# Kernel optimization log

Hardware: AMD Instinct MI355X
Metric: run time of the kernel (lower is better)

Reference implementation:

```python
import jax, jax.numpy as jnp
import numpy as np

EPS = 1e-5
D = 32          # token embedding dim
HEADS = 8
DH = D // HEADS  # 4


def _layernorm(x, g, b):
    mu = jnp.mean(x, axis=-1, keepdims=True)
    var = jnp.mean(jnp.square(x - mu), axis=-1, keepdims=True)
    return (x - mu) / jnp.sqrt(var + EPS) * g + b


def _mhsa(x, Wqvk, W0):
    # x: [..., t, 32]; Wqvk: [96, 32]; W0: [32, 32]
    qkv = x @ Wqvk.T                                   # [..., t, 96]
    qkv = qkv.reshape(qkv.shape[:-1] + (DH, 3, HEADS))  # (d k h) layout of original rearrange
    q, k, v = qkv[..., 0, :], qkv[..., 1, :], qkv[..., 2, :]  # [..., t, d, h]
    scores = jnp.einsum('...tdh,...sdh->...hts', q, k) * (DH ** -0.5)
    attn = jax.nn.softmax(scores, axis=-1)
    out = jnp.einsum('...hts,...sdh->...thd', attn, v)  # [..., t, h, d]
    out = out.reshape(out.shape[:-2] + (D,))            # (h d) concat order
    return out @ W0.T


def setup_inputs() -> dict:
    key = jax.random.key(0)
    ks = jax.random.split(key, 8)
    B = 256
    s = D ** -0.5
    return {
        'x':       jax.random.normal(ks[0], (B, 3, 32, 32, 32), dtype=jnp.float32),
        'pos_y':   jax.random.normal(ks[1], (3, 32, 32), dtype=jnp.float32) * s,
        'Wqvk_y':  jax.random.normal(ks[2], (3, 3 * D, D), dtype=jnp.float32) * s,
        'W0_y':    jax.random.normal(ks[3], (3, D, D), dtype=jnp.float32) * s,
        'g_y':     jnp.ones((D,), dtype=jnp.float32),
        'b_y':     jnp.zeros((D,), dtype=jnp.float32),
        'Wqvk_x':  jax.random.normal(ks[4], (3, 3 * D, D), dtype=jnp.float32) * s,
        'W0_x':    jax.random.normal(ks[5], (3, D, D), dtype=jnp.float32) * s,
        'g_x':     jnp.ones((D,), dtype=jnp.float32),
        'b_x':     jnp.zeros((D,), dtype=jnp.float32),
    }


def reference(x, pos_y, Wqvk_y, W0_y, g_y, b_y, Wqvk_x, W0_x, g_x, b_x):
    # x: [b, 3, l, w, h] with l=w=h=32. Dropout layers are in eval mode (identity).
    tst = jnp.transpose(x, (0, 1, 4, 2, 3))               # [b, 3, i(=h), t(=l), d(=w)]
    # AbsPosEmb1D per RGB channel: in_ @ pos^T
    emb = jnp.einsum('bcitd,cjd->bcitj', tst, pos_y)      # [b, 3, 32, 32, 32]
    outs = []
    for c in range(3):  # distinct r/g/b weights
        o = _mhsa(emb[:, c], Wqvk_y[c], W0_y[c])
        outs.append(_layernorm(emb[:, c] + o, g_y, b_y))
    x_tmp = jnp.stack(outs, axis=1)                       # [b, 3, i, t, 32]
    x_tmp = jnp.transpose(x_tmp, (0, 1, 3, 4, 2))         # [b, 3, t, 32, i]
    x1 = jax.nn.sigmoid(x_tmp) * x                        # first gating

    # BUG in original second loop: it reuses the stale `emb_y` from the last
    # iteration of the first loop (channel b, i = width-1) for every (i, j).
    emb_last = emb[:, 2, -1]                              # [b, 32, 32]
    ys = []
    for c in range(3):
        o = _mhsa(emb_last, Wqvk_x[c], W0_x[c])
        ys.append(_layernorm(emb_last + o, g_x, b_x))
    tmp2 = jnp.stack(ys, axis=1)                          # [b, 3, t, 32]
    # y stacked over i (constant across i), then permuted to [b,3,32,i,32]
    y_perm = jnp.transpose(tmp2, (0, 1, 3, 2))[:, :, :, None, :]  # [b,3,32,1,32]
    return jax.nn.sigmoid(y_perm) * x1
```

## Files before the change

kernel.cpp:

```cpp
#include <hip/hip_runtime.h>
#include <hip/hip_bf16.h>


using bf16 = __hip_bfloat16;
typedef float v2f __attribute__((ext_vector_type(2)));

__device__ __forceinline__ v2f pk_fma(v2f acc, v2f a, v2f b) {
  asm("v_pk_fma_f32 %0, %1, %2, %0" : "+v"(acc) : "v"(a), "v"(b));
  return acc;
}

struct __align__(16) SMem {
  float psJ[32][36];
  float wqF[96][34];
  float esw[32][36];
  float xs[32][34];
  float qS[32][34];
  float kT[32][36];
  float vT[32][36];
};

__device__ __forceinline__ void load_tables(
    SMem& sm, int tid, const float* __restrict__ xbc, int i,
    const float* __restrict__ pos, const float* __restrict__ wq,
    const float* __restrict__ g, const float* __restrict__ b)
{
  const int t = tid >> 3, dq = tid & 7;
  float xv0 = xbc[(t * 32 + dq * 4 + 0) * 32 + i];
  float xv1 = xbc[(t * 32 + dq * 4 + 1) * 32 + i];
  float xv2 = xbc[(t * 32 + dq * 4 + 2) * 32 + i];
  float xv3 = xbc[(t * 32 + dq * 4 + 3) * 32 + i];
  *(v2f*)&sm.xs[t][dq * 4]     = v2f{xv0, xv1};
  *(v2f*)&sm.xs[t][dq * 4 + 2] = v2f{xv2, xv3};
  {
    const int e = tid * 4;
    float4 p = *(const float4*)&pos[e];
    *(float4*)&sm.psJ[e >> 5][e & 31] = p;
  }
  {
    float wf[12];
    *(float4*)&wf[0] = *(const float4*)&wq[tid * 12];
    *(float4*)&wf[4] = *(const float4*)&wq[tid * 12 + 4];
    *(float4*)&wf[8] = *(const float4*)&wq[tid * 12 + 8];
#pragma unroll
    for (int k = 0; k < 6; ++k) {
      const int e = tid * 12 + 2 * k;
      *(v2f*)&sm.wqF[e >> 5][e & 31] = v2f{wf[2 * k], wf[2 * k + 1]};
    }
  }
  if (tid < 32) { sm.esw[tid][34] = g[tid]; sm.esw[tid][35] = b[tid]; }
}

__device__ __forceinline__ void mhsa_core(SMem& sm, int tid,
                                          const float* __restrict__ w0g,
                                          float sig_out[4])
{
  const int t = tid >> 3, j4 = tid & 7;
  float eres[4];

  {
    v2f acc[4] = {v2f{0.f,0.f}, v2f{0.f,0.f}, v2f{0.f,0.f}, v2f{0.f,0.f}};
#pragma unroll
    for (int d4 = 0; d4 < 8; ++d4) {
      v2f xa = *(const v2f*)&sm.xs[t][4 * d4];
      v2f xb = *(const v2f*)&sm.xs[t][4 * d4 + 2];
#pragma unroll
      for (int q = 0; q < 4; ++q) {
        float4 p4 = *(const float4*)&sm.psJ[j4 + 8 * q][4 * d4];
        acc[q] = pk_fma(acc[q], xa, v2f{p4.x, p4.y});
        acc[q] = pk_fma(acc[q], xb, v2f{p4.z, p4.w});
      }
    }
#pragma unroll
    for (int q = 0; q < 4; ++q) {
      eres[q] = acc[q][0] + acc[q][1];
      sm.esw[t][j4 + 8 * q] = eres[q];
    }
  }
  __syncthreads();

  {
    const int t0 = (tid >> 4) * 2, fg = tid & 15;
    float* sp[6]; int st[6];
#pragma unroll
    for (int m = 0; m < 6; ++m) {
      const int f = fg + 16 * m;
      const int dh = f / 24, r = f - 24 * dh;
      const int sel = r >> 3, cc = (r & 7) * 4 + dh;
      if (sel == 0)      { sp[m] = &sm.qS[0][0] + cc;      st[m] = 34; }
      else if (sel == 1) { sp[m] = &sm.kT[0][0] + cc * 36; st[m] = 1;  }
      else               { sp[m] = &sm.vT[0][0] + cc * 36; st[m] = 1;  }
    }
    v2f acc0[6], acc1[6];
#pragma unroll
    for (int m = 0; m < 6; ++m) { acc0[m] = v2f{0.f,0.f}; acc1[m] = v2f{0.f,0.f}; }
#pragma unroll
    for (int jb = 0; jb < 8; ++jb) {
      float4 e0 = *(const float4*)&sm.esw[t0][4 * jb];
      float4 e1 = *(const float4*)&sm.esw[t0 + 1][4 * jb];
      v2f e0a = v2f{e0.x, e0.y}, e0b = v2f{e0.z, e0.w};
      v2f e1a = v2f{e1.x, e1.y}, e1b = v2f{e1.z, e1.w};
#pragma unroll
      for (int m = 0; m < 6; ++m) {
        v2f wa = *(const v2f*)&sm.wqF[fg + 16 * m][4 * jb];
        v2f wb = *(const v2f*)&sm.wqF[fg + 16 * m][4 * jb + 2];
        acc0[m] = pk_fma(acc0[m], e0a, wa);
        acc0[m] = pk_fma(acc0[m], e0b, wb);
        acc1[m] = pk_fma(acc1[m], e1a, wa);
        acc1[m] = pk_fma(acc1[m], e1b, wb);
      }
    }
#pragma unroll
    for (int m = 0; m < 6; ++m) {
      sp[m][t0 * st[m]]       = acc0[m][0] + acc0[m][1];
      sp[m][(t0 + 1) * st[m]] = acc1[m][0] + acc1[m][1];
    }
  }
  __syncthreads();

  float4 w0v = *(const float4*)&w0g[tid * 4];

  {
    const int h = tid >> 5, tt = tid & 31;
    v2f qa = *(const v2f*)&sm.qS[tt][4 * h];
    v2f qb = *(const v2f*)&sm.qS[tt][4 * h + 2];
    v2f q0 = v2f{qa[0], qa[0]}, q1 = v2f{qa[1], qa[1]};
    v2f q2 = v2f{qb[0], qb[0]}, q3 = v2f{qb[1], qb[1]};
    const float* kr0 = &sm.kT[4 * h + 0][0];
    const float* kr1 = &sm.kT[4 * h + 1][0];
    const float* kr2 = &sm.kT[4 * h + 2][0];
    const float* kr3 = &sm.kT[4 * h + 3][0];
    v2f sc2[16];
#pragma unroll
    for (int s4 = 0; s4 < 8; ++s4) {
      float4 k0 = *(const float4*)&kr0[4 * s4];
      float4 k1 = *(const float4*)&kr1[4 * s4];
      float4 k2 = *(const float4*)&kr2[4 * s4];
      float4 k3 = *(const float4*)&kr3[4 * s4];
      v2f ea = v2f{0.f,0.f}, eb = v2f{0.f,0.f};
      ea = pk_fma(ea, q0, v2f{k0.x, k0.y}); eb = pk_fma(eb, q0, v2f{k0.z, k0.w});
      ea = pk_fma(ea, q1, v2f{k1.x, k1.y}); eb = pk_fma(eb, q1, v2f{k1.z, k1.w});
      ea = pk_fma(ea, q2, v2f{k2.x, k2.y}); eb = pk_fma(eb, q2, v2f{k2.z, k2.w});
      ea = pk_fma(ea, q3, v2f{k3.x, k3.y}); eb = pk_fma(eb, q3, v2f{k3.z, k3.w});
      sc2[2 * s4] = ea; sc2[2 * s4 + 1] = eb;
    }
    const float C = 0.72134752f;
    v2f den = v2f{0.f, 0.f};
#pragma unroll
    for (int s2 = 0; s2 < 16; ++s2) {
      sc2[s2][0] = exp2f(sc2[s2][0] * C);
      sc2[s2][1] = exp2f(sc2[s2][1] * C);
      den += sc2[s2];
    }
    const float inv = __fdividef(1.0f, den[0] + den[1]);
    const float* vr0 = &sm.vT[4 * h + 0][0];
    const float* vr1 = &sm.vT[4 * h + 1][0];
    const float* vr2 = &sm.vT[4 * h + 2][0];
    const float* vr3 = &sm.vT[4 * h + 3][0];
    v2f o0 = v2f{0.f,0.f}, o1 = v2f{0.f,0.f}, o2 = v2f{0.f,0.f}, o3 = v2f{0.f,0.f};
#pragma unroll
    for (int s4 = 0; s4 < 8; ++s4) {
      v2f aa = sc2[2 * s4], ab = sc2[2 * s4 + 1];
      float4 v0 = *(const float4*)&vr0[4 * s4];
      float4 v1 = *(const float4*)&vr1[4 * s4];
      float4 v2v = *(const float4*)&vr2[4 * s4];
      float4 v3 = *(const float4*)&vr3[4 * s4];
      o0 = pk_fma(o0, aa, v2f{v0.x, v0.y});  o0 = pk_fma(o0, ab, v2f{v0.z, v0.w});
      o1 = pk_fma(o1, aa, v2f{v1.x, v1.y});  o1 = pk_fma(o1, ab, v2f{v1.z, v1.w});
      o2 = pk_fma(o2, aa, v2f{v2v.x, v2v.y}); o2 = pk_fma(o2, ab, v2f{v2v.z, v2v.w});
      o3 = pk_fma(o3, aa, v2f{v3.x, v3.y});  o3 = pk_fma(o3, ab, v2f{v3.z, v3.w});
    }
    float4 ao;
    ao.x = (o0[0] + o0[1]) * inv;  ao.y = (o1[0] + o1[1]) * inv;
    ao.z = (o2[0] + o2[1]) * inv;  ao.w = (o3[0] + o3[1]) * inv;
    *(float4*)&sm.psJ[tt][4 * h] = ao;
  }
  {
    const int e = tid * 4;
    *(float4*)&sm.esw[e >> 5][e & 31] = w0v;
  }
  __syncthreads();

  {
    v2f acc[4] = {v2f{0.f,0.f}, v2f{0.f,0.f}, v2f{0.f,0.f}, v2f{0.f,0.f}};
#pragma unroll
    for (int f4 = 0; f4 < 8; ++f4) {
      float4 a4 = *(const float4*)&sm.psJ[t][4 * f4];
      v2f alo = v2f{a4.x, a4.y}, ahi = v2f{a4.z, a4.w};
#pragma unroll
      for (int q = 0; q < 4; ++q) {
        float4 w4 = *(const float4*)&sm.esw[j4 + 8 * q][4 * f4];
        acc[q] = pk_fma(acc[q], alo, v2f{w4.x, w4.y});
        acc[q] = pk_fma(acc[q], ahi, v2f{w4.z, w4.w});
      }
    }
    float rr[4];
    float s1 = 0.f, s2 = 0.f;
#pragma unroll
    for (int q = 0; q < 4; ++q) {
      rr[q] = acc[q][0] + acc[q][1] + eres[q];
      s1 += rr[q]; s2 += rr[q] * rr[q];
    }
#pragma unroll
    for (int m = 1; m < 8; m <<= 1) {
      s1 += __shfl_xor(s1, m, 64);
      s2 += __shfl_xor(s2, m, 64);
    }
    const float mu   = s1 * (1.0f / 32.0f);
    const float var  = s2 * (1.0f / 32.0f) - mu * mu;
    const float rstd = rsqrtf(var + 1e-5f);
    const float L2E  = 1.44269504f;
#pragma unroll
    for (int q = 0; q < 4; ++q) {
      const int j = j4 + 8 * q;
      const float z = (rr[q] - mu) * rstd * sm.esw[j][34] + sm.esw[j][35];
      sig_out[q] = __fdividef(1.0f, 1.0f + exp2f(-z * L2E));
    }
  }
}

__global__ __launch_bounds__(256, 4) void phase1_kernel(
    const float* __restrict__ x, const float* __restrict__ pos_y,
    const float* __restrict__ wqvk_x, const float* __restrict__ w0_x,
    const float* __restrict__ g_x, const float* __restrict__ b_x,
    bf16* __restrict__ gates)
{
  __shared__ SMem sm;
  const int tid = threadIdx.x;
  const int n = blockIdx.x;
  const int c = n % 3, b = n / 3;
  const float* xbc = x + (size_t)(b * 3 + 2) * 32768;
  load_tables(sm, tid, xbc, 31, pos_y + 2 * 1024, wqvk_x + c * 3072, g_x, b_x);
  __syncthreads();
  float sig[4];
  mhsa_core(sm, tid, w0_x + c * 1024, sig);
  const int t = tid >> 3, j4 = tid & 7;
#pragma unroll
  for (int q = 0; q < 4; ++q)
    gates[((c * 256 + b) * 32 + t) * 32 + j4 + 8 * q] = __float2bfloat16(sig[q]);
}

__global__ __launch_bounds__(256, 4) void phase2_kernel(
    const float* __restrict__ x, const float* __restrict__ pos_y,
    const float* __restrict__ wqvk_y, const float* __restrict__ w0_y,
    const float* __restrict__ g_y, const float* __restrict__ b_y,
    const bf16* __restrict__ gates, float* __restrict__ out)
{
  __shared__ SMem sm;
  const int tid = threadIdx.x;
  const int n = blockIdx.x;
  const int p = (n & 7) * 3072 + (n >> 3);
  const int i = p & 31, bc = p >> 5;
  const int c = bc % 3, b = bc / 3;
  const float* xbc = x + (size_t)bc * 32768;
  load_tables(sm, tid, xbc, i, pos_y + c * 1024, wqvk_y + c * 3072, g_y, b_y);
  if (tid < 32)
    sm.xs[tid][32] = __bfloat162float(gates[((c * 256 + b) * 32 + i) * 32 + tid]);
  __syncthreads();
  float sig[4];
  mhsa_core(sm, tid, w0_y + c * 1024, sig);
  const int t = tid >> 3, j4 = tid & 7;
  const float sgv = sm.xs[t][32];
  float* ob = out + (size_t)bc * 32768 + i;
#pragma unroll
  for (int q = 0; q < 4; ++q) {
    const int j = j4 + 8 * q;
    ob[(t * 32 + j) * 32] = sgv * sig[q] * sm.xs[t][j];
  }
}

extern "C" void kernel_launch(void* const* d_in, const int* in_sizes, int n_in,
                              void* d_out, int out_size, void* d_ws, size_t ws_size,
                              hipStream_t stream) {
  const float* x      = (const float*)d_in[0];
  const float* pos_y  = (const float*)d_in[1];
  const float* wqvk_y = (const float*)d_in[2];
  const float* w0_y   = (const float*)d_in[3];
  const float* g_y    = (const float*)d_in[4];
  const float* b_y    = (const float*)d_in[5];
  const float* wqvk_x = (const float*)d_in[6];
  const float* w0_x   = (const float*)d_in[7];
  const float* g_x    = (const float*)d_in[8];
  const float* b_x    = (const float*)d_in[9];
  bf16* gates = (bf16*)d_ws;

  hipLaunchKernelGGL(phase1_kernel, dim3(768), dim3(256), 0, stream,
                     x, pos_y, wqvk_x, w0_x, g_x, b_x, gates);
  hipLaunchKernelGGL(phase2_kernel, dim3(24576), dim3(256), 0, stream,
                     x, pos_y, wqvk_y, w0_y, g_y, b_y, gates, (float*)d_out);
}
```

Measured before the change: 463.8 us.

## Fold positional embedding into QKV weights and retile MHSA stages 2x2

A small precompute kernel multiplies Wqkv by the positional table, with the softmax scale folded into the Q rows, so QKV is computed directly from x. This lets the embedding and QKV stages run without a barrier between them, and the runtime softmax scale multiply is dropped. The embedding and output-projection matmuls are retiled to 2x2 outputs per thread. W0 is loaded up front into its own shared buffer, and the LayerNorm gain and bias are prescaled by log2e. The cost is an extra kernel launch and a different floating-point rounding order.

```diff
diff --git a/kernel.cpp b/kernel.cpp
--- a/kernel.cpp
+++ b/kernel.cpp
@@ -12,113 +12,158 @@
 
 struct __align__(16) SMem {
   float psJ[32][36];
-  float wqF[96][34];
-  float esw[32][36];
-  float xs[32][34];
+  float wcF[96][34];
+  float w0s[32][36];
+  float xs[32][36];
   float qS[32][34];
   float kT[32][36];
   float vT[32][36];
 };
 
+__global__ __launch_bounds__(256) void wc_kernel(
+    const float* __restrict__ pos_y, const float* __restrict__ wqvk_y,
+    const float* __restrict__ wqvk_x, float* __restrict__ wc)
+{
+  const int n = blockIdx.x;
+  const int c = n % 3, xset = n / 3;
+  const float* W = (xset ? wqvk_x : wqvk_y) + c * 3072;
+  const float* P = pos_y + (xset ? 2 : c) * 1024;
+  __shared__ float Ws[96][33];
+  __shared__ float Ps[32][33];
+  const int tid = threadIdx.x;
+#pragma unroll
+  for (int k = 0; k < 12; ++k) {
+    const int e = tid * 12 + k;
+    Ws[e >> 5][e & 31] = W[e];
+  }
+#pragma unroll
+  for (int k = 0; k < 4; ++k) {
+    const int e = tid * 4 + k;
+    Ps[e >> 5][e & 31] = P[e];
+  }
+  __syncthreads();
+  const int fg = tid >> 3, d0 = (tid & 7) * 4;
+#pragma unroll
+  for (int m = 0; m < 3; ++m) {
+    const int f = fg + 32 * m;
+    float s0 = 0.f, s1 = 0.f, s2 = 0.f, s3 = 0.f;
+#pragma unroll
+    for (int j = 0; j < 32; ++j) {
+      const float w = Ws[f][j];
+      s0 += w * Ps[j][d0];     s1 += w * Ps[j][d0 + 1];
+      s2 += w * Ps[j][d0 + 2]; s3 += w * Ps[j][d0 + 3];
+    }
+    const float sc = ((f % 24) < 8) ? 0.72134752f : 1.0f;
+    float* o = wc + (size_t)n * 3072 + f * 32 + d0;
+    o[0] = s0 * sc; o[1] = s1 * sc; o[2] = s2 * sc; o[3] = s3 * sc;
+  }
+}
+
 __device__ __forceinline__ void load_tables(
     SMem& sm, int tid, const float* __restrict__ xbc, int i,
-    const float* __restrict__ pos, const float* __restrict__ wq,
+    const float* __restrict__ pos, const float* __restrict__ wcg,
+    const float* __restrict__ w0g,
     const float* __restrict__ g, const float* __restrict__ b)
 {
-  const int t = tid >> 3, dq = tid & 7;
-  float xv0 = xbc[(t * 32 + dq * 4 + 0) * 32 + i];
-  float xv1 = xbc[(t * 32 + dq * 4 + 1) * 32 + i];
-  float xv2 = xbc[(t * 32 + dq * 4 + 2) * 32 + i];
-  float xv3 = xbc[(t * 32 + dq * 4 + 3) * 32 + i];
-  *(v2f*)&sm.xs[t][dq * 4]     = v2f{xv0, xv1};
-  *(v2f*)&sm.xs[t][dq * 4 + 2] = v2f{xv2, xv3};
+  const int t = tid >> 3, dq = (tid & 7) * 4;
+  float xv0 = xbc[(t * 32 + dq + 0) * 32 + i];
+  float xv1 = xbc[(t * 32 + dq + 1) * 32 + i];
+  float xv2 = xbc[(t * 32 + dq + 2) * 32 + i];
+  float xv3 = xbc[(t * 32 + dq + 3) * 32 + i];
+  *(float4*)&sm.xs[t][dq] = make_float4(xv0, xv1, xv2, xv3);
   {
     const int e = tid * 4;
     float4 p = *(const float4*)&pos[e];
     *(float4*)&sm.psJ[e >> 5][e & 31] = p;
+    float4 w = *(const float4*)&w0g[e];
+    *(float4*)&sm.w0s[e >> 5][e & 31] = w;
   }
   {
     float wf[12];
-    *(float4*)&wf[0] = *(const float4*)&wq[tid * 12];
-    *(float4*)&wf[4] = *(const float4*)&wq[tid * 12 + 4];
-    *(float4*)&wf[8] = *(const float4*)&wq[tid * 12 + 8];
+    *(float4*)&wf[0] = *(const float4*)&wcg[tid * 12];
+    *(float4*)&wf[4] = *(const float4*)&wcg[tid * 12 + 4];
+    *(float4*)&wf[8] = *(const float4*)&wcg[tid * 12 + 8];
 #pragma unroll
     for (int k = 0; k < 6; ++k) {
       const int e = tid * 12 + 2 * k;
-      *(v2f*)&sm.wqF[e >> 5][e & 31] = v2f{wf[2 * k], wf[2 * k + 1]};
-    }
-  }
-  if (tid < 32) { sm.esw[tid][34] = g[tid]; sm.esw[tid][35] = b[tid]; }
-}
-
-__device__ __forceinline__ void mhsa_core(SMem& sm, int tid,
-                                          const float* __restrict__ w0g,
-                                          float sig_out[4])
-{
-  const int t = tid >> 3, j4 = tid & 7;
-  float eres[4];
-
-  {
-    v2f acc[4] = {v2f{0.f,0.f}, v2f{0.f,0.f}, v2f{0.f,0.f}, v2f{0.f,0.f}};
+      *(v2f*)&sm.wcF[e >> 5][e & 31] = v2f{wf[2 * k], wf[2 * k + 1]};
+    }
+  }
+  if (tid < 32) {
+    sm.xs[tid][33] = g[tid] * 1.44269504f;
+    sm.xs[tid][34] = b[tid] * 1.44269504f;
+  }
+}
+
+__device__ __forceinline__ void mhsa_core(SMem& sm, int tid, float sig_out[2][2])
+{
+  const int te = (tid >> 4) * 2, je = (tid & 15) * 2;
+  float eres[2][2];
+
+  {
+    v2f a00{0.f,0.f}, a01{0.f,0.f}, a10{0.f,0.f}, a11{0.f,0.f};
 #pragma unroll
     for (int d4 = 0; d4 < 8; ++d4) {
-      v2f xa = *(const v2f*)&sm.xs[t][4 * d4];
-      v2f xb = *(const v2f*)&sm.xs[t][4 * d4 + 2];
-#pragma unroll
-      for (int q = 0; q < 4; ++q) {
-        float4 p4 = *(const float4*)&sm.psJ[j4 + 8 * q][4 * d4];
-        acc[q] = pk_fma(acc[q], xa, v2f{p4.x, p4.y});
-        acc[q] = pk_fma(acc[q], xb, v2f{p4.z, p4.w});
-      }
-    }
-#pragma unroll
-    for (int q = 0; q < 4; ++q) {
-      eres[q] = acc[q][0] + acc[q][1];
-      sm.esw[t][j4 + 8 * q] = eres[q];
-    }
-  }
-  __syncthreads();
-
-  {
-    const int t0 = (tid >> 4) * 2, fg = tid & 15;
-    float* sp[6]; int st[6];
-#pragma unroll
-    for (int m = 0; m < 6; ++m) {
-      const int f = fg + 16 * m;
-      const int dh = f / 24, r = f - 24 * dh;
-      const int sel = r >> 3, cc = (r & 7) * 4 + dh;
+      float4 x0 = *(const float4*)&sm.xs[te][4 * d4];
+      float4 x1 = *(const float4*)&sm.xs[te + 1][4 * d4];
+      float4 p0 = *(const float4*)&sm.psJ[je][4 * d4];
+      float4 p1 = *(const float4*)&sm.psJ[je + 1][4 * d4];
+      a00 = pk_fma(a00, v2f{x0.x, x0.y}, v2f{p0.x, p0.y});
+      a00 = pk_fma(a00, v2f{x0.z, x0.w}, v2f{p0.z, p0.w});
+      a01 = pk_fma(a01, v2f{x0.x, x0.y}, v2f{p1.x, p1.y});
+      a01 = pk_fma(a01, v2f{x0.z, x0.w}, v2f{p1.z, p1.w});
+      a10 = pk_fma(a10, v2f{x1.x, x1.y}, v2f{p0.x, p0.y});
+      a10 = pk_fma(a10, v2f{x1.z, x1.w}, v2f{p0.z, p0.w});
+      a11 = pk_fma(a11, v2f{x1.x, x1.y}, v2f{p1.x, p1.y});
+      a11 = pk_fma(a11, v2f{x1.z, x1.w}, v2f{p1.z, p1.w});
+    }
+    eres[0][0] = a00[0] + a00[1]; eres[0][1] = a01[0] + a01[1];
+    eres[1][0] = a10[0] + a10[1]; eres[1][1] = a11[0] + a11[1];
+  }
+  {
+    const int tg = (tid >> 5) * 4, rg = tid & 31;
+    float* sp[3]; int st[3];
+#pragma unroll
+    for (int m = 0; m < 3; ++m) {
+      const int f = rg + 32 * m;
+      const int dh = f / 24, r2 = f - 24 * dh;
+      const int sel = r2 >> 3, cc = (r2 & 7) * 4 + dh;
       if (sel == 0)      { sp[m] = &sm.qS[0][0] + cc;      st[m] = 34; }
       else if (sel == 1) { sp[m] = &sm.kT[0][0] + cc * 36; st[m] = 1;  }
       else               { sp[m] = &sm.vT[0][0] + cc * 36; st[m] = 1;  }
     }
-    v2f acc0[6], acc1[6];
-#pragma unroll
-    for (int m = 0; m < 6; ++m) { acc0[m] = v2f{0.f,0.f}; acc1[m] = v2f{0.f,0.f}; }
-#pragma unroll
-    for (int jb = 0; jb < 8; ++jb) {
-      float4 e0 = *(const float4*)&sm.esw[t0][4 * jb];
-      float4 e1 = *(const float4*)&sm.esw[t0 + 1][4 * jb];
-      v2f e0a = v2f{e0.x, e0.y}, e0b = v2f{e0.z, e0.w};
-      v2f e1a = v2f{e1.x, e1.y}, e1b = v2f{e1.z, e1.w};
-#pragma unroll
-      for (int m = 0; m < 6; ++m) {
-        v2f wa = *(const v2f*)&sm.wqF[fg + 16 * m][4 * jb];
-        v2f wb = *(const v2f*)&sm.wqF[fg + 16 * m][4 * jb + 2];
-        acc0[m] = pk_fma(acc0[m], e0a, wa);
-        acc0[m] = pk_fma(acc0[m], e0b, wb);
-        acc1[m] = pk_fma(acc1[m], e1a, wa);
-        acc1[m] = pk_fma(acc1[m], e1b, wb);
+    v2f acc[3][4];
+#pragma unroll
+    for (int m = 0; m < 3; ++m)
+#pragma unroll
+      for (int k = 0; k < 4; ++k) acc[m][k] = v2f{0.f, 0.f};
+#pragma unroll
+    for (int d4 = 0; d4 < 8; ++d4) {
+      float4 a0 = *(const float4*)&sm.xs[tg + 0][4 * d4];
+      float4 a1 = *(const float4*)&sm.xs[tg + 1][4 * d4];
+      float4 a2 = *(const float4*)&sm.xs[tg + 2][4 * d4];
+      float4 a3 = *(const float4*)&sm.xs[tg + 3][4 * d4];
+#pragma unroll
+      for (int m = 0; m < 3; ++m) {
+        v2f wlo = *(const v2f*)&sm.wcF[rg + 32 * m][4 * d4];
+        v2f whi = *(const v2f*)&sm.wcF[rg + 32 * m][4 * d4 + 2];
+        acc[m][0] = pk_fma(acc[m][0], v2f{a0.x, a0.y}, wlo);
+        acc[m][0] = pk_fma(acc[m][0], v2f{a0.z, a0.w}, whi);
+        acc[m][1] = pk_fma(acc[m][1], v2f{a1.x, a1.y}, wlo);
+        acc[m][1] = pk_fma(acc[m][1], v2f{a1.z, a1.w}, whi);
+        acc[m][2] = pk_fma(acc[m][2], v2f{a2.x, a2.y}, wlo);
+        acc[m][2] = pk_fma(acc[m][2], v2f{a2.z, a2.w}, whi);
+        acc[m][3] = pk_fma(acc[m][3], v2f{a3.x, a3.y}, wlo);
+        acc[m][3] = pk_fma(acc[m][3], v2f{a3.z, a3.w}, whi);
       }
     }
 #pragma unroll
-    for (int m = 0; m < 6; ++m) {
-      sp[m][t0 * st[m]]       = acc0[m][0] + acc0[m][1];
-      sp[m][(t0 + 1) * st[m]] = acc1[m][0] + acc1[m][1];
-    }
-  }
-  __syncthreads();
-
-  float4 w0v = *(const float4*)&w0g[tid * 4];
+    for (int m = 0; m < 3; ++m)
+#pragma unroll
+      for (int k = 0; k < 4; ++k)
+        sp[m][(tg + k) * st[m]] = acc[m][k][0] + acc[m][k][1];
+  }
+  __syncthreads();
 
   {
     const int h = tid >> 5, tt = tid & 31;
@@ -137,19 +182,18 @@
       float4 k1 = *(const float4*)&kr1[4 * s4];
       float4 k2 = *(const float4*)&kr2[4 * s4];
       float4 k3 = *(const float4*)&kr3[4 * s4];
-      v2f ea = v2f{0.f,0.f}, eb = v2f{0.f,0.f};
+      v2f ea = v2f{0.f, 0.f}, eb = v2f{0.f, 0.f};
       ea = pk_fma(ea, q0, v2f{k0.x, k0.y}); eb = pk_fma(eb, q0, v2f{k0.z, k0.w});
       ea = pk_fma(ea, q1, v2f{k1.x, k1.y}); eb = pk_fma(eb, q1, v2f{k1.z, k1.w});
       ea = pk_fma(ea, q2, v2f{k2.x, k2.y}); eb = pk_fma(eb, q2, v2f{k2.z, k2.w});
       ea = pk_fma(ea, q3, v2f{k3.x, k3.y}); eb = pk_fma(eb, q3, v2f{k3.z, k3.w});
       sc2[2 * s4] = ea; sc2[2 * s4 + 1] = eb;
     }
-    const float C = 0.72134752f;
     v2f den = v2f{0.f, 0.f};
 #pragma unroll
     for (int s2 = 0; s2 < 16; ++s2) {
-      sc2[s2][0] = exp2f(sc2[s2][0] * C);
-      sc2[s2][1] = exp2f(sc2[s2][1] * C);
+      sc2[s2][0] = exp2f(sc2[s2][0]);
+      sc2[s2][1] = exp2f(sc2[s2][1]);
       den += sc2[s2];
     }
     const float inv = __fdividef(1.0f, den[0] + den[1]);
@@ -165,63 +209,65 @@
       float4 v1 = *(const float4*)&vr1[4 * s4];
       float4 v2v = *(const float4*)&vr2[4 * s4];
       float4 v3 = *(const float4*)&vr3[4 * s4];
-      o0 = pk_fma(o0, aa, v2f{v0.x, v0.y});  o0 = pk_fma(o0, ab, v2f{v0.z, v0.w});
-      o1 = pk_fma(o1, aa, v2f{v1.x, v1.y});  o1 = pk_fma(o1, ab, v2f{v1.z, v1.w});
+      o0 = pk_fma(o0, aa, v2f{v0.x, v0.y});   o0 = pk_fma(o0, ab, v2f{v0.z, v0.w});
+      o1 = pk_fma(o1, aa, v2f{v1.x, v1.y});   o1 = pk_fma(o1, ab, v2f{v1.z, v1.w});
       o2 = pk_fma(o2, aa, v2f{v2v.x, v2v.y}); o2 = pk_fma(o2, ab, v2f{v2v.z, v2v.w});
-      o3 = pk_fma(o3, aa, v2f{v3.x, v3.y});  o3 = pk_fma(o3, ab, v2f{v3.z, v3.w});
+      o3 = pk_fma(o3, aa, v2f{v3.x, v3.y});   o3 = pk_fma(o3, ab, v2f{v3.z, v3.w});
     }
     float4 ao;
     ao.x = (o0[0] + o0[1]) * inv;  ao.y = (o1[0] + o1[1]) * inv;
     ao.z = (o2[0] + o2[1]) * inv;  ao.w = (o3[0] + o3[1]) * inv;
     *(float4*)&sm.psJ[tt][4 * h] = ao;
   }
-  {
-    const int e = tid * 4;
-    *(float4*)&sm.esw[e >> 5][e & 31] = w0v;
-  }
-  __syncthreads();
-
-  {
-    v2f acc[4] = {v2f{0.f,0.f}, v2f{0.f,0.f}, v2f{0.f,0.f}, v2f{0.f,0.f}};
+  __syncthreads();
+
+  {
+    v2f a00{0.f,0.f}, a01{0.f,0.f}, a10{0.f,0.f}, a11{0.f,0.f};
 #pragma unroll
     for (int f4 = 0; f4 < 8; ++f4) {
-      float4 a4 = *(const float4*)&sm.psJ[t][4 * f4];
-      v2f alo = v2f{a4.x, a4.y}, ahi = v2f{a4.z, a4.w};
-#pragma unroll
-      for (int q = 0; q < 4; ++q) {
-        float4 w4 = *(const float4*)&sm.esw[j4 + 8 * q][4 * f4];
-        acc[q] = pk_fma(acc[q], alo, v2f{w4.x, w4.y});
-        acc[q] = pk_fma(acc[q], ahi, v2f{w4.z, w4.w});
-      }
-    }
-    float rr[4];
-    float s1 = 0.f, s2 = 0.f;
-#pragma unroll
-    for (int q = 0; q < 4; ++q) {
-      rr[q] = acc[q][0] + acc[q][1] + eres[q];
-      s1 += rr[q]; s2 += rr[q] * rr[q];
-    }
-#pragma unroll
-    for (int m = 1; m < 8; m <<= 1) {
-      s1 += __shfl_xor(s1, m, 64);
-      s2 += __shfl_xor(s2, m, 64);
-    }
-    const float mu   = s1 * (1.0f / 32.0f);
-    const float var  = s2 * (1.0f / 32.0f) - mu * mu;
-    const float rstd = rsqrtf(var + 1e-5f);
-    const float L2E  = 1.44269504f;
-#pragma unroll
-    for (int q = 0; q < 4; ++q) {
-      const int j = j4 + 8 * q;
-      const float z = (rr[q] - mu) * rstd * sm.esw[j][34] + sm.esw[j][35];
-      sig_out[q] = __fdividef(1.0f, 1.0f + exp2f(-z * L2E));
-    }
+      float4 u0 = *(const float4*)&sm.psJ[te][4 * f4];
+      float4 u1 = *(const float4*)&sm.psJ[te + 1][4 * f4];
+      float4 w0 = *(const float4*)&sm.w0s[je][4 * f4];
+      float4 w1 = *(const float4*)&sm.w0s[je + 1][4 * f4];
+      a00 = pk_fma(a00, v2f{u0.x, u0.y}, v2f{w0.x, w0.y});
+      a00 = pk_fma(a00, v2f{u0.z, u0.w}, v2f{w0.z, w0.w});
+      a01 = pk_fma(a01, v2f{u0.x, u0.y}, v2f{w1.x, w1.y});
+      a01 = pk_fma(a01, v2f{u0.z, u0.w}, v2f{w1.z, w1.w});
+      a10 = pk_fma(a10, v2f{u1.x, u1.y}, v2f{w0.x, w0.y});
+      a10 = pk_fma(a10, v2f{u1.z, u1.w}, v2f{w0.z, w0.w});
+      a11 = pk_fma(a11, v2f{u1.x, u1.y}, v2f{w1.x, w1.y});
+      a11 = pk_fma(a11, v2f{u1.z, u1.w}, v2f{w1.z, w1.w});
+    }
+    float rr[2][2];
+    rr[0][0] = a00[0] + a00[1] + eres[0][0];
+    rr[0][1] = a01[0] + a01[1] + eres[0][1];
+    rr[1][0] = a10[0] + a10[1] + eres[1][0];
+    rr[1][1] = a11[0] + a11[1] + eres[1][1];
+    float s1a = rr[0][0] + rr[0][1], s1b = rr[1][0] + rr[1][1];
+    float s2a = rr[0][0]*rr[0][0] + rr[0][1]*rr[0][1];
+    float s2b = rr[1][0]*rr[1][0] + rr[1][1]*rr[1][1];
+#pragma unroll
+    for (int m = 1; m < 16; m <<= 1) {
+      s1a += __shfl_xor(s1a, m, 64);
+      s2a += __shfl_xor(s2a, m, 64);
+      s1b += __shfl_xor(s1b, m, 64);
+      s2b += __shfl_xor(s2b, m, 64);
+    }
+    const float mua = s1a * (1.0f / 32.0f), mub = s1b * (1.0f / 32.0f);
+    const float ra = rsqrtf(s2a * (1.0f / 32.0f) - mua * mua + 1e-5f);
+    const float rb = rsqrtf(s2b * (1.0f / 32.0f) - mub * mub + 1e-5f);
+    const float g0 = sm.xs[je][33],     b0 = sm.xs[je][34];
+    const float g1 = sm.xs[je + 1][33], b1 = sm.xs[je + 1][34];
+    sig_out[0][0] = __fdividef(1.0f, 1.0f + exp2f(-((rr[0][0] - mua) * ra * g0 + b0)));
+    sig_out[0][1] = __fdividef(1.0f, 1.0f + exp2f(-((rr[0][1] - mua) * ra * g1 + b1)));
+    sig_out[1][0] = __fdividef(1.0f, 1.0f + exp2f(-((rr[1][0] - mub) * rb * g0 + b0)));
+    sig_out[1][1] = __fdividef(1.0f, 1.0f + exp2f(-((rr[1][1] - mub) * rb * g1 + b1)));
   }
 }
 
 __global__ __launch_bounds__(256, 4) void phase1_kernel(
     const float* __restrict__ x, const float* __restrict__ pos_y,
-    const float* __restrict__ wqvk_x, const float* __restrict__ w0_x,
+    const float* __restrict__ wc, const float* __restrict__ w0_x,
     const float* __restrict__ g_x, const float* __restrict__ b_x,
     bf16* __restrict__ gates)
 {
@@ -230,19 +276,22 @@
   const int n = blockIdx.x;
   const int c = n % 3, b = n / 3;
   const float* xbc = x + (size_t)(b * 3 + 2) * 32768;
-  load_tables(sm, tid, xbc, 31, pos_y + 2 * 1024, wqvk_x + c * 3072, g_x, b_x);
-  __syncthreads();
-  float sig[4];
-  mhsa_core(sm, tid, w0_x + c * 1024, sig);
-  const int t = tid >> 3, j4 = tid & 7;
-#pragma unroll
-  for (int q = 0; q < 4; ++q)
-    gates[((c * 256 + b) * 32 + t) * 32 + j4 + 8 * q] = __float2bfloat16(sig[q]);
+  load_tables(sm, tid, xbc, 31, pos_y + 2 * 1024,
+              wc + (size_t)(3 + c) * 3072, w0_x + c * 1024, g_x, b_x);
+  __syncthreads();
+  float sig[2][2];
+  mhsa_core(sm, tid, sig);
+  const int te = (tid >> 4) * 2, je = (tid & 15) * 2;
+#pragma unroll
+  for (int u = 0; u < 2; ++u)
+#pragma unroll
+    for (int v = 0; v < 2; ++v)
+      gates[((c * 256 + b) * 32 + te + u) * 32 + je + v] = __float2bfloat16(sig[u][v]);
 }
 
 __global__ __launch_bounds__(256, 4) void phase2_kernel(
     const float* __restrict__ x, const float* __restrict__ pos_y,
-    const float* __restrict__ wqvk_y, const float* __restrict__ w0_y,
+    const float* __restrict__ wc, const float* __restrict__ w0_y,
     const float* __restrict__ g_y, const float* __restrict__ b_y,
     const bf16* __restrict__ gates, float* __restrict__ out)
 {
@@ -253,19 +302,21 @@
   const int i = p & 31, bc = p >> 5;
   const int c = bc % 3, b = bc / 3;
   const float* xbc = x + (size_t)bc * 32768;
-  load_tables(sm, tid, xbc, i, pos_y + c * 1024, wqvk_y + c * 3072, g_y, b_y);
+  load_tables(sm, tid, xbc, i, pos_y + c * 1024,
+              wc + (size_t)c * 3072, w0_y + c * 1024, g_y, b_y);
   if (tid < 32)
     sm.xs[tid][32] = __bfloat162float(gates[((c * 256 + b) * 32 + i) * 32 + tid]);
   __syncthreads();
-  float sig[4];
-  mhsa_core(sm, tid, w0_y + c * 1024, sig);
-  const int t = tid >> 3, j4 = tid & 7;
-  const float sgv = sm.xs[t][32];
+  float sig[2][2];
+  mhsa_core(sm, tid, sig);
+  const int te = (tid >> 4) * 2, je = (tid & 15) * 2;
   float* ob = out + (size_t)bc * 32768 + i;
 #pragma unroll
-  for (int q = 0; q < 4; ++q) {
-    const int j = j4 + 8 * q;
-    ob[(t * 32 + j) * 32] = sgv * sig[q] * sm.xs[t][j];
+  for (int u = 0; u < 2; ++u) {
+    const float sgv = sm.xs[te + u][32];
+#pragma unroll
+    for (int v = 0; v < 2; ++v)
+      ob[((te + u) * 32 + je + v) * 32] = sgv * sig[u][v] * sm.xs[te + u][je + v];
   }
 }
 
@@ -282,10 +333,13 @@
   const float* w0_x   = (const float*)d_in[7];
   const float* g_x    = (const float*)d_in[8];
   const float* b_x    = (const float*)d_in[9];
-  bf16* gates = (bf16*)d_ws;
-
+  bf16*  gates = (bf16*)d_ws;
+  float* wcbuf = (float*)((char*)d_ws + 1572864);
+
+  hipLaunchKernelGGL(wc_kernel, dim3(6), dim3(256), 0, stream,
+                     pos_y, wqvk_y, wqvk_x, wcbuf);
   hipLaunchKernelGGL(phase1_kernel, dim3(768), dim3(256), 0, stream,
-                     x, pos_y, wqvk_x, w0_x, g_x, b_x, gates);
+                     x, pos_y, wcbuf, w0_x, g_x, b_x, gates);
   hipLaunchKernelGGL(phase2_kernel, dim3(24576), dim3(256), 0, stream,
-                     x, pos_y, wqvk_y, w0_y, g_y, b_y, gates, (float*)d_out);
-}
+                     x, pos_y, wcbuf, w0_y, g_y, b_y, gates, (float*)d_out);
+}
```

After: 463.6 us. About the same (-0.1%).
